# Kernel optimization log

Measured on AMD Instinct MI355X. Metric: run time of the kernel, lower is better.

## Reference

```python
import jax, jax.numpy as jnp
import numpy as np

HID = 160
SUB = HID // 5  # 32

def leaky_relu(x):
    return jnp.where(x > 0, x, 0.01 * x)

def sage_conv(x, src, dst, W_l, b_l, W_r, n_nodes):
    # PyG SAGEConv(mean): out = lin_l(mean_{j in N(i)} x_j) + lin_r(x_i)
    msg_sum = jax.ops.segment_sum(x[src], dst, num_segments=n_nodes)
    deg = jax.ops.segment_sum(jnp.ones((src.shape[0], 1), x.dtype), dst, num_segments=n_nodes)
    mean = msg_sum / jnp.maximum(deg, 1.0)
    return mean @ W_l + b_l + x @ W_r

def setup_inputs() -> dict:
    key = jax.random.key(0)
    ks = jax.random.split(key, 32)
    N, E, LM = 50000, 500000, 768
    inp = {
        "x": jax.random.normal(ks[0], (N, LM), jnp.float32),
        "edge_index": jax.random.randint(ks[1], (2, E), 0, N, jnp.int64),
        "num_prop": jax.random.normal(ks[2], (N, 6), jnp.float32),
        "num_category": jax.random.normal(ks[3], (N, 11), jnp.float32),
        "des_tensor": jax.random.normal(ks[4], (N, LM), jnp.float32),
        "tweet_tensor": jax.random.normal(ks[5], (N, LM), jnp.float32),
    }
    def lin(k, fin, fout):
        s = 1.0 / np.sqrt(fin)
        kw, kb = jax.random.split(k)
        return (jax.random.uniform(kw, (fin, fout), jnp.float32, -s, s),
                jax.random.uniform(kb, (fout,), jnp.float32, -s, s))
    inp["W_des"], inp["b_des"] = lin(ks[6], LM, SUB)
    inp["W_tw"], inp["b_tw"] = lin(ks[7], LM, SUB)
    inp["W_txt"], inp["b_txt"] = lin(ks[8], LM, SUB)
    inp["W_np"], inp["b_np"] = lin(ks[9], 6, SUB)
    inp["W_nc"], inp["b_nc"] = lin(ks[10], 11, SUB)
    inp["W_in"], inp["b_in"] = lin(ks[11], HID, HID)
    inp["W_l"], inp["b_l"] = lin(ks[12], HID, HID)
    inp["W_r"], _ = lin(ks[13], HID, HID)  # lin_r has no bias in PyG SAGEConv
    inp["W_o1"], inp["b_o1"] = lin(ks[14], HID, HID)
    inp["W_o2"], inp["b_o2"] = lin(ks[15], HID, 2)
    return inp

def reference(x, edge_index, num_prop, num_category, des_tensor, tweet_tensor,
              W_des, b_des, W_tw, b_tw, W_txt, b_txt, W_np, b_np, W_nc, b_nc,
              W_in, b_in, W_l, b_l, W_r, W_o1, b_o1, W_o2, b_o2):
    # dropout in eval mode (identity)
    n_nodes = x.shape[0]
    src, dst = edge_index[0], edge_index[1]
    d = leaky_relu(des_tensor @ W_des + b_des)
    tw = leaky_relu(tweet_tensor @ W_tw + b_tw)
    t = leaky_relu(x @ W_txt + b_txt)
    n = leaky_relu(num_prop @ W_np + b_np)
    c = leaky_relu(num_category @ W_nc + b_nc)
    h = jnp.concatenate((n, c, d, tw, t), axis=1)  # [N, 160]
    h = leaky_relu(h @ W_in + b_in)
    h = sage_conv(h, src, dst, W_l, b_l, W_r, n_nodes)  # conv1 applied twice (shared weights)
    h = sage_conv(h, src, dst, W_l, b_l, W_r, n_nodes)
    em = leaky_relu(h @ W_o1 + b_o1)
    out = em @ W_o2 + b_o2
    return (out, em)
```

## Files before the change

kernel.cpp:

```cpp
#include <hip/hip_runtime.h>
#include <hip/hip_bf16.h>

#define HID 160
#define LM 768

__device__ __forceinline__ float leaky(float x) { return x > 0.0f ? x : 0.01f * x; }

__global__ __launch_bounds__(256) void count_deg_kernel(const int* __restrict__ ei, int* __restrict__ deg, int E) {
    int e = blockIdx.x * 256 + threadIdx.x;
    if (e < E) atomicAdd(&deg[ei[E + e]], 1);
}

__global__ __launch_bounds__(1024) void scan_kernel(const int* __restrict__ deg, int* __restrict__ rowstart,
                                                    float* __restrict__ invd, int N) {
    __shared__ int wsum[16];
    __shared__ int carry_s;
    int t = threadIdx.x;
    int lane = t & 63;
    int w = t >> 6;
    if (t == 0) carry_s = 0;
    __syncthreads();
    for (int base = 0; base < N; base += 1024) {
        int i = base + t;
        int v = (i < N) ? deg[i] : 0;
        int x = v;
        #pragma unroll
        for (int off = 1; off < 64; off <<= 1) {
            int y = __shfl_up(x, off);
            x = (lane >= off) ? x + y : x;
        }
        if (lane == 63) wsum[w] = x;
        __syncthreads();
        int woff = 0;
        for (int k = 0; k < w; k++) woff += wsum[k];
        int excl = carry_s + woff + x - v;
        if (i < N) {
            rowstart[i] = excl;
            invd[i] = 1.0f / (float)(v > 0 ? v : 1);
        }
        __syncthreads();
        if (t == 1023) carry_s += woff + x;
        __syncthreads();
    }
}

__global__ __launch_bounds__(256) void fill_csr_kernel(const int* __restrict__ ei, const int* __restrict__ rowstart,
                                                       int* __restrict__ cursor, int* __restrict__ csr, int E) {
    int e = blockIdx.x * 256 + threadIdx.x;
    if (e < E) {
        int d = ei[E + e];
        int p = atomicAdd(&cursor[d], 1);
        csr[rowstart[d] + p] = ei[e];
    }
}

#define ETM 64
__global__ __launch_bounds__(256, 4) void enc768_kernel(
    const float* __restrict__ des, const float* __restrict__ twt, const float* __restrict__ xx,
    const float* __restrict__ Wd, const float* __restrict__ Wt, const float* __restrict__ Wx,
    const float* __restrict__ bd, const float* __restrict__ bt, const float* __restrict__ bx,
    float* __restrict__ H0, int N) {
    __shared__ float As[ETM * 68];
    __shared__ float Ws[64 * 36];
    int t = threadIdx.x;
    int z = blockIdx.z;
    const float* A = z == 0 ? des : (z == 1 ? twt : xx);
    const float* W = z == 0 ? Wd : (z == 1 ? Wt : Wx);
    const float* b = z == 0 ? bd : (z == 1 ? bt : bx);
    int colOff = 64 + 32 * z;
    int b0 = blockIdx.x * ETM;
    int rg = t & 31, cg = t >> 5;
    float acc0[4] = {};
    float acc1[4] = {};
    for (int kb = 0; kb < LM; kb += 64) {
        __syncthreads();
        #pragma unroll
        for (int i = 0; i < 4; i++) {
            int f = t + 256 * i;
            int row = f >> 4, kq = f & 15;
            int gr = b0 + row;
            float4 v = make_float4(0.f, 0.f, 0.f, 0.f);
            if (gr < N) v = *(const float4*)(A + (size_t)gr * LM + kb + 4 * kq);
            *(float4*)(&As[row * 68 + 4 * kq]) = v;
        }
        #pragma unroll
        for (int i = 0; i < 2; i++) {
            int f = t + 256 * i;
            int row = f >> 3, q = f & 7;
            *(float4*)(&Ws[row * 36 + 4 * q]) = *(const float4*)(W + (size_t)(kb + row) * 32 + 4 * q);
        }
        __syncthreads();
        #pragma unroll
        for (int k4 = 0; k4 < 16; k4++) {
            float4 a0 = *(const float4*)(&As[rg * 68 + 4 * k4]);
            float4 a1 = *(const float4*)(&As[(rg + 32) * 68 + 4 * k4]);
            float a0v[4] = {a0.x, a0.y, a0.z, a0.w};
            float a1v[4] = {a1.x, a1.y, a1.z, a1.w};
            #pragma unroll
            for (int j = 0; j < 4; j++) {
                float4 w = *(const float4*)(&Ws[(4 * k4 + j) * 36 + 4 * cg]);
                acc0[0] += a0v[j] * w.x; acc0[1] += a0v[j] * w.y;
                acc0[2] += a0v[j] * w.z; acc0[3] += a0v[j] * w.w;
                acc1[0] += a1v[j] * w.x; acc1[1] += a1v[j] * w.y;
                acc1[2] += a1v[j] * w.z; acc1[3] += a1v[j] * w.w;
            }
        }
    }
    float4 bv = *(const float4*)(b + 4 * cg);
    int gr0 = b0 + rg;
    if (gr0 < N) {
        float4 o;
        o.x = leaky(acc0[0] + bv.x); o.y = leaky(acc0[1] + bv.y);
        o.z = leaky(acc0[2] + bv.z); o.w = leaky(acc0[3] + bv.w);
        *(float4*)(H0 + (size_t)gr0 * HID + colOff + 4 * cg) = o;
    }
    int gr1 = b0 + rg + 32;
    if (gr1 < N) {
        float4 o;
        o.x = leaky(acc1[0] + bv.x); o.y = leaky(acc1[1] + bv.y);
        o.z = leaky(acc1[2] + bv.z); o.w = leaky(acc1[3] + bv.w);
        *(float4*)(H0 + (size_t)gr1 * HID + colOff + 4 * cg) = o;
    }
}

__global__ __launch_bounds__(256) void enc_small_kernel(
    const float* __restrict__ npr, const float* __restrict__ ncat,
    const float* __restrict__ Wnp, const float* __restrict__ bnp,
    const float* __restrict__ Wnc, const float* __restrict__ bnc,
    float* __restrict__ H0, int N) {
    __shared__ float sWnp[192], sbnp[32], sWnc[352], sbnc[32];
    int t = threadIdx.x;
    if (t < 192) sWnp[t] = Wnp[t];
    for (int i = t; i < 352; i += 256) sWnc[i] = Wnc[i];
    if (t < 32) { sbnp[t] = bnp[t]; sbnc[t] = bnc[t]; }
    __syncthreads();
    int i = blockIdx.x * 256 + t;
    if (i >= N) return;
    float a[11];
    #pragma unroll
    for (int j = 0; j < 6; j++) a[j] = npr[(size_t)i * 6 + j];
    float o[32];
    #pragma unroll
    for (int c = 0; c < 32; c++) {
        float s = sbnp[c];
        #pragma unroll
        for (int j = 0; j < 6; j++) s += a[j] * sWnp[j * 32 + c];
        o[c] = leaky(s);
    }
    #pragma unroll
    for (int q = 0; q < 8; q++)
        *(float4*)(H0 + (size_t)i * HID + 4 * q) = make_float4(o[4 * q], o[4 * q + 1], o[4 * q + 2], o[4 * q + 3]);
    #pragma unroll
    for (int j = 0; j < 11; j++) a[j] = ncat[(size_t)i * 11 + j];
    #pragma unroll
    for (int c = 0; c < 32; c++) {
        float s = sbnc[c];
        #pragma unroll
        for (int j = 0; j < 11; j++) s += a[j] * sWnc[j * 32 + c];
        o[c] = leaky(s);
    }
    #pragma unroll
    for (int q = 0; q < 8; q++)
        *(float4*)(H0 + (size_t)i * HID + 32 + 4 * q) = make_float4(o[4 * q], o[4 * q + 1], o[4 * q + 2], o[4 * q + 3]);
}

template <bool DUAL, bool ACT>
__global__ __launch_bounds__(256) void gemm160_kernel(
    const float* __restrict__ A1, const float* __restrict__ W1,
    const float* __restrict__ A2, const float* __restrict__ W2,
    const float* __restrict__ bias, float* __restrict__ C, int N) {
    __shared__ float As[64 * 33];
    __shared__ float Ws[32 * 160];
    int t = threadIdx.x;
    int b0 = blockIdx.x * 64;
    int rg = t & 15, cg = t >> 4;
    float acc[4][10] = {};
    const int NC = DUAL ? 10 : 5;
    for (int c = 0; c < NC; c++) {
        const float* A = (c < 5) ? A1 : A2;
        const float* W = (c < 5) ? W1 : W2;
        int kb = 32 * (c % 5);
        __syncthreads();
        #pragma unroll
        for (int i = 0; i < 2; i++) {
            int f = t + 256 * i;
            int row = f >> 3, kq = f & 7;
            int gr = b0 + row;
            float4 v = make_float4(0.f, 0.f, 0.f, 0.f);
            if (gr < N) v = *(const float4*)(A + (size_t)gr * HID + kb + 4 * kq);
            As[row * 33 + 4 * kq + 0] = v.x;
            As[row * 33 + 4 * kq + 1] = v.y;
            As[row * 33 + 4 * kq + 2] = v.z;
            As[row * 33 + 4 * kq + 3] = v.w;
        }
        #pragma unroll
        for (int i = 0; i < 5; i++) {
            int f = t + 256 * i;
            int row = f / 40, q = f % 40;
            *(float4*)(Ws + row * 160 + 4 * q) = *(const float4*)(W + (size_t)(kb + row) * 160 + 4 * q);
        }
        __syncthreads();
        #pragma unroll 4
        for (int kk = 0; kk < 32; kk++) {
            float a[4];
            #pragma unroll
            for (int i = 0; i < 4; i++) a[i] = As[(rg + 16 * i) * 33 + kk];
            const float2* wp = (const float2*)(Ws + kk * 160 + 10 * cg);
            #pragma unroll
            for (int j = 0; j < 5; j++) {
                float2 w = wp[j];
                #pragma unroll
                for (int i = 0; i < 4; i++) {
                    acc[i][2 * j + 0] += a[i] * w.x;
                    acc[i][2 * j + 1] += a[i] * w.y;
                }
            }
        }
    }
    float bv[10];
    #pragma unroll
    for (int j = 0; j < 10; j++) bv[j] = bias[10 * cg + j];
    #pragma unroll
    for (int i = 0; i < 4; i++) {
        int gr = b0 + rg + 16 * i;
        if (gr < N) {
            float* Cr = C + (size_t)gr * HID + 10 * cg;
            #pragma unroll
            for (int j = 0; j < 5; j++) {
                float vx = acc[i][2 * j + 0] + bv[2 * j + 0];
                float vy = acc[i][2 * j + 1] + bv[2 * j + 1];
                if (ACT) { vx = leaky(vx); vy = leaky(vy); }
                *(float2*)(Cr + 2 * j) = make_float2(vx, vy);
            }
        }
    }
}

__global__ __launch_bounds__(256) void agg_kernel(const float* __restrict__ H,
                                                  const int* __restrict__ rowstart, const int* __restrict__ deg,
                                                  const int* __restrict__ csr, const float* __restrict__ invd,
                                                  float* __restrict__ M, int N) {
    int wid = (blockIdx.x * 256 + threadIdx.x) >> 6;
    int lane = threadIdx.x & 63;
    if (wid >= N) return;
    int rs = rowstart[wid];
    int d = deg[wid];
    float inv = invd[wid];
    if (lane < 40) {
        float4 acc = make_float4(0.f, 0.f, 0.f, 0.f);
        const float4* Hv = (const float4*)H;
        for (int j = 0; j < d; j++) {
            int s = csr[rs + j];
            float4 v = Hv[(size_t)s * 40 + lane];
            acc.x += v.x; acc.y += v.y; acc.z += v.z; acc.w += v.w;
        }
        float4 o = make_float4(acc.x * inv, acc.y * inv, acc.z * inv, acc.w * inv);
        ((float4*)M)[(size_t)wid * 40 + lane] = o;
    }
}

__global__ __launch_bounds__(256) void out_head_kernel(const float* __restrict__ em,
                                                       const float* __restrict__ Wo2, const float* __restrict__ bo2,
                                                       float* __restrict__ out, int N) {
    __shared__ float sW[320];
    __shared__ float sb[2];
    int t = threadIdx.x;
    for (int i = t; i < 320; i += 256) sW[i] = Wo2[i];
    if (t < 2) sb[t] = bo2[t];
    __syncthreads();
    int i = blockIdx.x * 256 + t;
    if (i >= N) return;
    const float4* er = (const float4*)em + (size_t)i * 40;
    float ax = sb[0], ay = sb[1];
    #pragma unroll 4
    for (int q = 0; q < 40; q++) {
        float4 v = er[q];
        int k = 8 * q;
        ax += v.x * sW[k + 0] + v.y * sW[k + 2] + v.z * sW[k + 4] + v.w * sW[k + 6];
        ay += v.x * sW[k + 1] + v.y * sW[k + 3] + v.z * sW[k + 5] + v.w * sW[k + 7];
    }
    out[2 * i + 0] = ax;
    out[2 * i + 1] = ay;
}

extern "C" void kernel_launch(void* const* d_in, const int* in_sizes, int n_in,
                              void* d_out, int out_size, void* d_ws, size_t ws_size,
                              hipStream_t stream) {
    const float* x        = (const float*)d_in[0];
    const int*   ei       = (const int*)d_in[1];
    const float* num_prop = (const float*)d_in[2];
    const float* num_cat  = (const float*)d_in[3];
    const float* des      = (const float*)d_in[4];
    const float* twt      = (const float*)d_in[5];
    const float* W_des = (const float*)d_in[6],  *b_des = (const float*)d_in[7];
    const float* W_tw  = (const float*)d_in[8],  *b_tw  = (const float*)d_in[9];
    const float* W_txt = (const float*)d_in[10], *b_txt = (const float*)d_in[11];
    const float* W_np  = (const float*)d_in[12], *b_np  = (const float*)d_in[13];
    const float* W_nc  = (const float*)d_in[14], *b_nc  = (const float*)d_in[15];
    const float* W_in  = (const float*)d_in[16], *b_in  = (const float*)d_in[17];
    const float* W_l   = (const float*)d_in[18], *b_l   = (const float*)d_in[19];
    const float* W_r   = (const float*)d_in[20];
    const float* W_o1  = (const float*)d_in[21], *b_o1  = (const float*)d_in[22];
    const float* W_o2  = (const float*)d_in[23], *b_o2  = (const float*)d_in[24];

    const int N = in_sizes[0] / LM;
    const int E = in_sizes[1] / 2;

    float* bufA = (float*)d_ws;
    float* bufB = bufA + (size_t)N * HID;
    int* deg      = (int*)(bufB + (size_t)N * HID);
    int* cursor   = deg + N;
    int* rowstart = cursor + N;
    float* invd   = (float*)(rowstart + N);
    int* csr      = (int*)(invd + N);

    float* out_ptr = (float*)d_out;
    float* em_ptr  = out_ptr + (size_t)N * 2;

    hipMemsetAsync(deg, 0, sizeof(int) * (size_t)(2 * N), stream);
    count_deg_kernel<<<(E + 255) / 256, 256, 0, stream>>>(ei, deg, E);
    scan_kernel<<<1, 1024, 0, stream>>>(deg, rowstart, invd, N);
    fill_csr_kernel<<<(E + 255) / 256, 256, 0, stream>>>(ei, rowstart, cursor, csr, E);

    dim3 egrid((N + ETM - 1) / ETM, 1, 3);
    enc768_kernel<<<egrid, 256, 0, stream>>>(des, twt, x, W_des, W_tw, W_txt, b_des, b_tw, b_txt, bufA, N);
    enc_small_kernel<<<(N + 255) / 256, 256, 0, stream>>>(num_prop, num_cat, W_np, b_np, W_nc, b_nc, bufA, N);

    int g64 = (N + 63) / 64;
    gemm160_kernel<false, true><<<g64, 256, 0, stream>>>(bufA, W_in, nullptr, nullptr, b_in, bufB, N);
    agg_kernel<<<(N + 3) / 4, 256, 0, stream>>>(bufB, rowstart, deg, csr, invd, bufA, N);
    gemm160_kernel<true, false><<<g64, 256, 0, stream>>>(bufA, W_l, bufB, W_r, b_l, bufA, N);
    agg_kernel<<<(N + 3) / 4, 256, 0, stream>>>(bufA, rowstart, deg, csr, invd, bufB, N);
    gemm160_kernel<true, false><<<g64, 256, 0, stream>>>(bufB, W_l, bufA, W_r, b_l, bufB, N);
    gemm160_kernel<false, true><<<g64, 256, 0, stream>>>(bufB, W_o1, nullptr, nullptr, b_o1, em_ptr, N);
    out_head_kernel<<<(N + 255) / 256, 256, 0, stream>>>(em_ptr, W_o2, b_o2, out_ptr, N);
}
```

Baseline: 1.019 ms.

## Read GEMM weights via wave-uniform scalar loads instead of shared memory tiles

Both the 768-wide encoder GEMM and the 160-wide GEMM kernels stop staging weights in shared memory. Each wave instead owns a column slice, chosen through readfirstlane so the weight loads are wave-uniform and can go through scalar loads. Row tiles double to 128 rows per block, with each lane computing two rows. This is meant to cut LDS traffic and sync overhead for weights and raise work per thread, but it adds many accumulators (80 in gemm160), which risks register pressure and spills and lowers occupancy.

```diff
diff --git a/kernel.cpp b/kernel.cpp
--- a/kernel.cpp
+++ b/kernel.cpp
@@ -54,14 +54,13 @@
     }
 }
 
-#define ETM 64
+#define ETM 128
 __global__ __launch_bounds__(256, 4) void enc768_kernel(
     const float* __restrict__ des, const float* __restrict__ twt, const float* __restrict__ xx,
     const float* __restrict__ Wd, const float* __restrict__ Wt, const float* __restrict__ Wx,
     const float* __restrict__ bd, const float* __restrict__ bt, const float* __restrict__ bx,
     float* __restrict__ H0, int N) {
     __shared__ float As[ETM * 68];
-    __shared__ float Ws[64 * 36];
     int t = threadIdx.x;
     int z = blockIdx.z;
     const float* A = z == 0 ? des : (z == 1 ? twt : xx);
@@ -69,13 +68,14 @@
     const float* b = z == 0 ? bd : (z == 1 ? bt : bx);
     int colOff = 64 + 32 * z;
     int b0 = blockIdx.x * ETM;
-    int rg = t & 31, cg = t >> 5;
-    float acc0[4] = {};
-    float acc1[4] = {};
+    int lane = t & 63;
+    int wq = __builtin_amdgcn_readfirstlane(t >> 6);
+    float acc0[8] = {};
+    float acc1[8] = {};
     for (int kb = 0; kb < LM; kb += 64) {
         __syncthreads();
         #pragma unroll
-        for (int i = 0; i < 4; i++) {
+        for (int i = 0; i < 8; i++) {
             int f = t + 256 * i;
             int row = f >> 4, kq = f & 15;
             int gr = b0 + row;
@@ -83,43 +83,47 @@
             if (gr < N) v = *(const float4*)(A + (size_t)gr * LM + kb + 4 * kq);
             *(float4*)(&As[row * 68 + 4 * kq]) = v;
         }
-        #pragma unroll
-        for (int i = 0; i < 2; i++) {
-            int f = t + 256 * i;
-            int row = f >> 3, q = f & 7;
-            *(float4*)(&Ws[row * 36 + 4 * q]) = *(const float4*)(W + (size_t)(kb + row) * 32 + 4 * q);
-        }
-        __syncthreads();
-        #pragma unroll
+        __syncthreads();
+        #pragma unroll 4
         for (int k4 = 0; k4 < 16; k4++) {
-            float4 a0 = *(const float4*)(&As[rg * 68 + 4 * k4]);
-            float4 a1 = *(const float4*)(&As[(rg + 32) * 68 + 4 * k4]);
+            float4 a0 = *(const float4*)(&As[lane * 68 + 4 * k4]);
+            float4 a1 = *(const float4*)(&As[(lane + 64) * 68 + 4 * k4]);
             float a0v[4] = {a0.x, a0.y, a0.z, a0.w};
             float a1v[4] = {a1.x, a1.y, a1.z, a1.w};
             #pragma unroll
             for (int j = 0; j < 4; j++) {
-                float4 w = *(const float4*)(&Ws[(4 * k4 + j) * 36 + 4 * cg]);
-                acc0[0] += a0v[j] * w.x; acc0[1] += a0v[j] * w.y;
-                acc0[2] += a0v[j] * w.z; acc0[3] += a0v[j] * w.w;
-                acc1[0] += a1v[j] * w.x; acc1[1] += a1v[j] * w.y;
-                acc1[2] += a1v[j] * w.z; acc1[3] += a1v[j] * w.w;
+                const float* Wk = W + (size_t)(kb + 4 * k4 + j) * 32 + 8 * wq;
+                #pragma unroll
+                for (int c = 0; c < 8; c++) {
+                    float wv = Wk[c];
+                    acc0[c] += a0v[j] * wv;
+                    acc1[c] += a1v[j] * wv;
+                }
             }
         }
     }
-    float4 bv = *(const float4*)(b + 4 * cg);
-    int gr0 = b0 + rg;
+    const float* bp = b + 8 * wq;
+    int gr0 = b0 + lane;
     if (gr0 < N) {
+        float* Hr = H0 + (size_t)gr0 * HID + colOff + 8 * wq;
         float4 o;
-        o.x = leaky(acc0[0] + bv.x); o.y = leaky(acc0[1] + bv.y);
-        o.z = leaky(acc0[2] + bv.z); o.w = leaky(acc0[3] + bv.w);
-        *(float4*)(H0 + (size_t)gr0 * HID + colOff + 4 * cg) = o;
-    }
-    int gr1 = b0 + rg + 32;
+        o.x = leaky(acc0[0] + bp[0]); o.y = leaky(acc0[1] + bp[1]);
+        o.z = leaky(acc0[2] + bp[2]); o.w = leaky(acc0[3] + bp[3]);
+        *(float4*)(Hr) = o;
+        o.x = leaky(acc0[4] + bp[4]); o.y = leaky(acc0[5] + bp[5]);
+        o.z = leaky(acc0[6] + bp[6]); o.w = leaky(acc0[7] + bp[7]);
+        *(float4*)(Hr + 4) = o;
+    }
+    int gr1 = b0 + lane + 64;
     if (gr1 < N) {
+        float* Hr = H0 + (size_t)gr1 * HID + colOff + 8 * wq;
         float4 o;
-        o.x = leaky(acc1[0] + bv.x); o.y = leaky(acc1[1] + bv.y);
-        o.z = leaky(acc1[2] + bv.z); o.w = leaky(acc1[3] + bv.w);
-        *(float4*)(H0 + (size_t)gr1 * HID + colOff + 4 * cg) = o;
+        o.x = leaky(acc1[0] + bp[0]); o.y = leaky(acc1[1] + bp[1]);
+        o.z = leaky(acc1[2] + bp[2]); o.w = leaky(acc1[3] + bp[3]);
+        *(float4*)(Hr) = o;
+        o.x = leaky(acc1[4] + bp[4]); o.y = leaky(acc1[5] + bp[5]);
+        o.z = leaky(acc1[6] + bp[6]); o.w = leaky(acc1[7] + bp[7]);
+        *(float4*)(Hr + 4) = o;
     }
 }
 
@@ -169,69 +173,74 @@
     const float* __restrict__ A1, const float* __restrict__ W1,
     const float* __restrict__ A2, const float* __restrict__ W2,
     const float* __restrict__ bias, float* __restrict__ C, int N) {
-    __shared__ float As[64 * 33];
-    __shared__ float Ws[32 * 160];
-    int t = threadIdx.x;
-    int b0 = blockIdx.x * 64;
-    int rg = t & 15, cg = t >> 4;
-    float acc[4][10] = {};
-    const int NC = DUAL ? 10 : 5;
-    for (int c = 0; c < NC; c++) {
-        const float* A = (c < 5) ? A1 : A2;
-        const float* W = (c < 5) ? W1 : W2;
-        int kb = 32 * (c % 5);
-        __syncthreads();
-        #pragma unroll
-        for (int i = 0; i < 2; i++) {
-            int f = t + 256 * i;
-            int row = f >> 3, kq = f & 7;
-            int gr = b0 + row;
-            float4 v = make_float4(0.f, 0.f, 0.f, 0.f);
-            if (gr < N) v = *(const float4*)(A + (size_t)gr * HID + kb + 4 * kq);
-            As[row * 33 + 4 * kq + 0] = v.x;
-            As[row * 33 + 4 * kq + 1] = v.y;
-            As[row * 33 + 4 * kq + 2] = v.z;
-            As[row * 33 + 4 * kq + 3] = v.w;
-        }
-        #pragma unroll
-        for (int i = 0; i < 5; i++) {
-            int f = t + 256 * i;
-            int row = f / 40, q = f % 40;
-            *(float4*)(Ws + row * 160 + 4 * q) = *(const float4*)(W + (size_t)(kb + row) * 160 + 4 * q);
-        }
-        __syncthreads();
-        #pragma unroll 4
-        for (int kk = 0; kk < 32; kk++) {
-            float a[4];
+    __shared__ float As[128 * 36];
+    int t = threadIdx.x;
+    int b0 = blockIdx.x * 128;
+    int lane = t & 63;
+    int wq = __builtin_amdgcn_readfirstlane(t >> 6);
+    float acc0[40] = {};
+    float acc1[40] = {};
+    const int NP = DUAL ? 2 : 1;
+    for (int p = 0; p < NP; p++) {
+        const float* A = (p == 0) ? A1 : A2;
+        const float* W = (p == 0) ? W1 : W2;
+        for (int kb = 0; kb < HID; kb += 32) {
+            __syncthreads();
             #pragma unroll
-            for (int i = 0; i < 4; i++) a[i] = As[(rg + 16 * i) * 33 + kk];
-            const float2* wp = (const float2*)(Ws + kk * 160 + 10 * cg);
-            #pragma unroll
-            for (int j = 0; j < 5; j++) {
-                float2 w = wp[j];
+            for (int i = 0; i < 4; i++) {
+                int f = t + 256 * i;
+                int row = f >> 3, kq = f & 7;
+                int gr = b0 + row;
+                float4 v = make_float4(0.f, 0.f, 0.f, 0.f);
+                if (gr < N) v = *(const float4*)(A + (size_t)gr * HID + kb + 4 * kq);
+                *(float4*)(&As[row * 36 + 4 * kq]) = v;
+            }
+            __syncthreads();
+            for (int k4 = 0; k4 < 8; k4++) {
+                float4 a0 = *(const float4*)(&As[lane * 36 + 4 * k4]);
+                float4 a1 = *(const float4*)(&As[(lane + 64) * 36 + 4 * k4]);
+                float a0v[4] = {a0.x, a0.y, a0.z, a0.w};
+                float a1v[4] = {a1.x, a1.y, a1.z, a1.w};
                 #pragma unroll
-                for (int i = 0; i < 4; i++) {
-                    acc[i][2 * j + 0] += a[i] * w.x;
-                    acc[i][2 * j + 1] += a[i] * w.y;
+                for (int j = 0; j < 4; j++) {
+                    const float* Wk = W + (size_t)(kb + 4 * k4 + j) * HID + 40 * wq;
+                    #pragma unroll
+                    for (int c = 0; c < 40; c++) {
+                        float wv = Wk[c];
+                        acc0[c] += a0v[j] * wv;
+                        acc1[c] += a1v[j] * wv;
+                    }
                 }
             }
         }
     }
-    float bv[10];
-    #pragma unroll
-    for (int j = 0; j < 10; j++) bv[j] = bias[10 * cg + j];
-    #pragma unroll
-    for (int i = 0; i < 4; i++) {
-        int gr = b0 + rg + 16 * i;
-        if (gr < N) {
-            float* Cr = C + (size_t)gr * HID + 10 * cg;
-            #pragma unroll
-            for (int j = 0; j < 5; j++) {
-                float vx = acc[i][2 * j + 0] + bv[2 * j + 0];
-                float vy = acc[i][2 * j + 1] + bv[2 * j + 1];
-                if (ACT) { vx = leaky(vx); vy = leaky(vy); }
-                *(float2*)(Cr + 2 * j) = make_float2(vx, vy);
-            }
+    const float* bp = bias + 40 * wq;
+    int gr0 = b0 + lane;
+    if (gr0 < N) {
+        float* Cr = C + (size_t)gr0 * HID + 40 * wq;
+        #pragma unroll
+        for (int q = 0; q < 10; q++) {
+            float4 o;
+            o.x = acc0[4 * q + 0] + bp[4 * q + 0];
+            o.y = acc0[4 * q + 1] + bp[4 * q + 1];
+            o.z = acc0[4 * q + 2] + bp[4 * q + 2];
+            o.w = acc0[4 * q + 3] + bp[4 * q + 3];
+            if (ACT) { o.x = leaky(o.x); o.y = leaky(o.y); o.z = leaky(o.z); o.w = leaky(o.w); }
+            *(float4*)(Cr + 4 * q) = o;
+        }
+    }
+    int gr1 = b0 + lane + 64;
+    if (gr1 < N) {
+        float* Cr = C + (size_t)gr1 * HID + 40 * wq;
+        #pragma unroll
+        for (int q = 0; q < 10; q++) {
+            float4 o;
+            o.x = acc1[4 * q + 0] + bp[4 * q + 0];
+            o.y = acc1[4 * q + 1] + bp[4 * q + 1];
+            o.z = acc1[4 * q + 2] + bp[4 * q + 2];
+            o.w = acc1[4 * q + 3] + bp[4 * q + 3];
+            if (ACT) { o.x = leaky(o.x); o.y = leaky(o.y); o.z = leaky(o.z); o.w = leaky(o.w); }
+            *(float4*)(Cr + 4 * q) = o;
         }
     }
 }
@@ -326,12 +335,12 @@
     enc768_kernel<<<egrid, 256, 0, stream>>>(des, twt, x, W_des, W_tw, W_txt, b_des, b_tw, b_txt, bufA, N);
     enc_small_kernel<<<(N + 255) / 256, 256, 0, stream>>>(num_prop, num_cat, W_np, b_np, W_nc, b_nc, bufA, N);
 
-    int g64 = (N + 63) / 64;
-    gemm160_kernel<false, true><<<g64, 256, 0, stream>>>(bufA, W_in, nullptr, nullptr, b_in, bufB, N);
+    int g128 = (N + 127) / 128;
+    gemm160_kernel<false, true><<<g128, 256, 0, stream>>>(bufA, W_in, nullptr, nullptr, b_in, bufB, N);
     agg_kernel<<<(N + 3) / 4, 256, 0, stream>>>(bufB, rowstart, deg, csr, invd, bufA, N);
-    gemm160_kernel<true, false><<<g64, 256, 0, stream>>>(bufA, W_l, bufB, W_r, b_l, bufA, N);
+    gemm160_kernel<true, false><<<g128, 256, 0, stream>>>(bufA, W_l, bufB, W_r, b_l, bufA, N);
     agg_kernel<<<(N + 3) / 4, 256, 0, stream>>>(bufA, rowstart, deg, csr, invd, bufB, N);
-    gemm160_kernel<true, false><<<g64, 256, 0, stream>>>(bufB, W_l, bufA, W_r, b_l, bufB, N);
-    gemm160_kernel<false, true><<<g64, 256, 0, stream>>>(bufB, W_o1, nullptr, nullptr, b_o1, em_ptr, N);
+    gemm160_kernel<true, false><<<g128, 256, 0, stream>>>(bufB, W_l, bufA, W_r, b_l, bufB, N);
+    gemm160_kernel<false, true><<<g128, 256, 0, stream>>>(bufB, W_o1, nullptr, nullptr, b_o1, em_ptr, N);
     out_head_kernel<<<(N + 255) / 256, 256, 0, stream>>>(em_ptr, W_o2, b_o2, out_ptr, N);
 }
```

Measured after the change: 1.193 ms. +17.1%, slower.

## Retile 768-wide encoder GEMM to 8x8 register tiles with 64-thread blocks

Applied to the files above, without the earlier changes.

Restructures the three text-encoder projections (N×768 @ 768×32) so each thread computes an 8-row by 8-column register tile, with 128-row blocks of 64 threads and a K step of 32. This raises arithmetic per shared-memory load and cuts LDS traffic per FMA compared with the previous 2x4 per-thread tile. In exchange it uses far fewer threads per block and more registers (64 accumulators), which lowers occupancy and latency hiding for a kernel that mostly streams about 460MB of input. The grid shrinks to about 1173 blocks.

```diff
diff --git a/kernel.cpp b/kernel.cpp
--- a/kernel.cpp
+++ b/kernel.cpp
@@ -54,14 +54,14 @@
     }
 }
 
-#define ETM 64
-__global__ __launch_bounds__(256, 4) void enc768_kernel(
+#define ETM 128
+__global__ __launch_bounds__(64, 2) void enc768_kernel(
     const float* __restrict__ des, const float* __restrict__ twt, const float* __restrict__ xx,
     const float* __restrict__ Wd, const float* __restrict__ Wt, const float* __restrict__ Wx,
     const float* __restrict__ bd, const float* __restrict__ bt, const float* __restrict__ bx,
     float* __restrict__ H0, int N) {
-    __shared__ float As[ETM * 68];
-    __shared__ float Ws[64 * 36];
+    __shared__ float As[ETM * 36];
+    __shared__ float Ws[32 * 36];
     int t = threadIdx.x;
     int z = blockIdx.z;
     const float* A = z == 0 ? des : (z == 1 ? twt : xx);
@@ -69,57 +69,66 @@
     const float* b = z == 0 ? bd : (z == 1 ? bt : bx);
     int colOff = 64 + 32 * z;
     int b0 = blockIdx.x * ETM;
-    int rg = t & 31, cg = t >> 5;
-    float acc0[4] = {};
-    float acc1[4] = {};
-    for (int kb = 0; kb < LM; kb += 64) {
-        __syncthreads();
-        #pragma unroll
-        for (int i = 0; i < 4; i++) {
-            int f = t + 256 * i;
-            int row = f >> 4, kq = f & 15;
+    int rg = t >> 2;
+    int cg = t & 3;
+    float acc[8][8] = {};
+    for (int kb = 0; kb < LM; kb += 32) {
+        __syncthreads();
+        #pragma unroll
+        for (int i = 0; i < 16; i++) {
+            int f = t + 64 * i;
+            int row = f >> 3, q = f & 7;
             int gr = b0 + row;
             float4 v = make_float4(0.f, 0.f, 0.f, 0.f);
-            if (gr < N) v = *(const float4*)(A + (size_t)gr * LM + kb + 4 * kq);
-            *(float4*)(&As[row * 68 + 4 * kq]) = v;
-        }
-        #pragma unroll
-        for (int i = 0; i < 2; i++) {
-            int f = t + 256 * i;
-            int row = f >> 3, q = f & 7;
-            *(float4*)(&Ws[row * 36 + 4 * q]) = *(const float4*)(W + (size_t)(kb + row) * 32 + 4 * q);
-        }
-        __syncthreads();
-        #pragma unroll
-        for (int k4 = 0; k4 < 16; k4++) {
-            float4 a0 = *(const float4*)(&As[rg * 68 + 4 * k4]);
-            float4 a1 = *(const float4*)(&As[(rg + 32) * 68 + 4 * k4]);
-            float a0v[4] = {a0.x, a0.y, a0.z, a0.w};
-            float a1v[4] = {a1.x, a1.y, a1.z, a1.w};
+            if (gr < N) v = *(const float4*)(A + (size_t)gr * LM + kb + 4 * q);
+            *(float4*)(&As[row * 36 + 4 * q]) = v;
+        }
+        #pragma unroll
+        for (int i = 0; i < 4; i++) {
+            int f = t + 64 * i;
+            int wr = f >> 3, q = f & 7;
+            *(float4*)(&Ws[wr * 36 + 4 * q]) = *(const float4*)(W + (size_t)(kb + wr) * 32 + 4 * q);
+        }
+        __syncthreads();
+        #pragma unroll
+        for (int k4 = 0; k4 < 8; k4++) {
+            float4 a[8];
+            #pragma unroll
+            for (int r = 0; r < 8; r++) a[r] = *(const float4*)(&As[(8 * rg + r) * 36 + 4 * k4]);
+            float4 w0[4], w1[4];
             #pragma unroll
             for (int j = 0; j < 4; j++) {
-                float4 w = *(const float4*)(&Ws[(4 * k4 + j) * 36 + 4 * cg]);
-                acc0[0] += a0v[j] * w.x; acc0[1] += a0v[j] * w.y;
-                acc0[2] += a0v[j] * w.z; acc0[3] += a0v[j] * w.w;
-                acc1[0] += a1v[j] * w.x; acc1[1] += a1v[j] * w.y;
-                acc1[2] += a1v[j] * w.z; acc1[3] += a1v[j] * w.w;
+                w0[j] = *(const float4*)(&Ws[(4 * k4 + j) * 36 + 8 * cg]);
+                w1[j] = *(const float4*)(&Ws[(4 * k4 + j) * 36 + 8 * cg + 4]);
             }
-        }
-    }
-    float4 bv = *(const float4*)(b + 4 * cg);
-    int gr0 = b0 + rg;
-    if (gr0 < N) {
-        float4 o;
-        o.x = leaky(acc0[0] + bv.x); o.y = leaky(acc0[1] + bv.y);
-        o.z = leaky(acc0[2] + bv.z); o.w = leaky(acc0[3] + bv.w);
-        *(float4*)(H0 + (size_t)gr0 * HID + colOff + 4 * cg) = o;
-    }
-    int gr1 = b0 + rg + 32;
-    if (gr1 < N) {
-        float4 o;
-        o.x = leaky(acc1[0] + bv.x); o.y = leaky(acc1[1] + bv.y);
-        o.z = leaky(acc1[2] + bv.z); o.w = leaky(acc1[3] + bv.w);
-        *(float4*)(H0 + (size_t)gr1 * HID + colOff + 4 * cg) = o;
+            #pragma unroll
+            for (int j = 0; j < 4; j++) {
+                #pragma unroll
+                for (int r = 0; r < 8; r++) {
+                    float av = (j == 0) ? a[r].x : (j == 1) ? a[r].y : (j == 2) ? a[r].z : a[r].w;
+                    acc[r][0] += av * w0[j].x; acc[r][1] += av * w0[j].y;
+                    acc[r][2] += av * w0[j].z; acc[r][3] += av * w0[j].w;
+                    acc[r][4] += av * w1[j].x; acc[r][5] += av * w1[j].y;
+                    acc[r][6] += av * w1[j].z; acc[r][7] += av * w1[j].w;
+                }
+            }
+        }
+    }
+    float4 bv0 = *(const float4*)(b + 8 * cg);
+    float4 bv1 = *(const float4*)(b + 8 * cg + 4);
+    #pragma unroll
+    for (int r = 0; r < 8; r++) {
+        int gr = b0 + 8 * rg + r;
+        if (gr < N) {
+            float* Hr = H0 + (size_t)gr * HID + colOff + 8 * cg;
+            float4 o;
+            o.x = leaky(acc[r][0] + bv0.x); o.y = leaky(acc[r][1] + bv0.y);
+            o.z = leaky(acc[r][2] + bv0.z); o.w = leaky(acc[r][3] + bv0.w);
+            *(float4*)(Hr) = o;
+            o.x = leaky(acc[r][4] + bv1.x); o.y = leaky(acc[r][5] + bv1.y);
+            o.z = leaky(acc[r][6] + bv1.z); o.w = leaky(acc[r][7] + bv1.w);
+            *(float4*)(Hr + 4) = o;
+        }
     }
 }
 
@@ -323,7 +332,7 @@
     fill_csr_kernel<<<(E + 255) / 256, 256, 0, stream>>>(ei, rowstart, cursor, csr, E);
 
     dim3 egrid((N + ETM - 1) / ETM, 1, 3);
-    enc768_kernel<<<egrid, 256, 0, stream>>>(des, twt, x, W_des, W_tw, W_txt, b_des, b_tw, b_txt, bufA, N);
+    enc768_kernel<<<egrid, 64, 0, stream>>>(des, twt, x, W_des, W_tw, W_txt, b_des, b_tw, b_txt, bufA, N);
     enc_small_kernel<<<(N + 255) / 256, 256, 0, stream>>>(num_prop, num_cat, W_np, b_np, W_nc, b_nc, bufA, N);
 
     int g64 = (N + 63) / 64;
```

New measurement: 1.353 ms. 32.8% more time.
